# Kernel optimization log

Measured on AMD Instinct MI355X. Metric: run time of the kernel, lower is better.

Reference implementation:

```python
import jax, jax.numpy as jnp
import numpy as np

B, N, HID = 1, 2048, 1024
H, WK, WV = 16, 64, 64
DH = HID // H  # 64


def setup_inputs() -> dict:
    key = jax.random.key(0)
    ks = jax.random.split(key, 10)
    s = 0.02
    return {
        "hidden_states": jax.random.normal(ks[0], (B, N, HID), jnp.float32),
        "attention_mask": jnp.ones((B, N), jnp.float32),
        "Wq": jax.random.normal(ks[1], (HID, HID), jnp.float32) * s,
        "bq": jnp.zeros((HID,), jnp.float32),
        "Wk": jax.random.normal(ks[2], (HID, HID), jnp.float32) * s,
        "bk": jnp.zeros((HID,), jnp.float32),
        "Wv": jax.random.normal(ks[3], (HID, HID), jnp.float32) * s,
        "bv": jnp.zeros((HID,), jnp.float32),
        # Conv1D(2*WK+1, DH, bias=False): weight [nx=DH, nf=2*WK+1]
        "W_rel_k": jax.random.normal(ks[4], (DH, 2 * WK + 1), jnp.float32) * s,
        # relative_pos_val: [2*WV+1, DH]
        "W_rel_v": jax.random.normal(ks[5], (2 * WV + 1, DH), jnp.float32) * s,
    }


def _attention(hidden_states, attention_mask, Wq, bq, Wk, bk, Wv, bv, W_rel_k, W_rel_v):
    b, n, _ = hidden_states.shape

    def heads(x):  # [B,N,HID] -> [B,H,N,DH]
        return x.reshape(b, n, H, DH).transpose(0, 2, 1, 3)

    q = heads(hidden_states @ Wq + bq)
    k = heads(hidden_states @ Wk + bk)
    v = heads(hidden_states @ Wv + bv)

    scores = jnp.einsum("bhid,bhjd->bhij", q, k)  # [B,H,N,N]

    # --- relative-position key bias: bias[i, j] = q_i . w_{j-i+WK} for |j-i|<=WK ---
    a_k = jnp.einsum("bhid,dw->bhiw", q, W_rel_k)  # [B,H,N,2*WK+1]
    rows = jnp.arange(n)
    slot = rows[None, :] - rows[:, None] + WK       # [N,N] relative slot j-i+WK
    valid_k = (slot >= 0) & (slot <= 2 * WK)
    bias = a_k[:, :, rows[:, None], jnp.clip(slot, 0, 2 * WK)]  # [B,H,N,N]
    scores = scores + jnp.where(valid_k, bias, 0.0)

    scores = scores / np.float32(np.sqrt(DH))  # temperature == 1.0

    # extended attention mask: (1 - mask) * dtype_min added to scores
    ext = (1.0 - attention_mask)[:, None, None, :] * jnp.finfo(scores.dtype).min
    scores = scores + ext

    probs = jax.nn.softmax(scores, axis=-1)  # [B,H,N,N]

    ctx = jnp.einsum("bhij,bhjd->bhid", probs, v)  # [B,H,N,DH]

    # --- relative-position value: band[i, r] = probs[i, i-WV+r]; ctx += band @ W_rel_v ---
    offs = jnp.arange(2 * WV + 1)
    kpos = rows[:, None] - WV + offs[None, :]       # [N, 2*WV+1] absolute key position
    valid_v = (kpos >= 0) & (kpos < n)
    band = probs[:, :, rows[:, None], jnp.clip(kpos, 0, n - 1)]  # [B,H,N,2*WV+1]
    band = jnp.where(valid_v, band, 0.0)
    ctx = ctx + jnp.einsum("bhiw,wd->bhid", band, W_rel_v)

    # merge heads -> [B,N,HID]
    return ctx.transpose(0, 2, 1, 3).reshape(b, n, HID)


def reference(hidden_states, attention_mask, Wq, bq, Wk, bk, Wv, bv, W_rel_k, W_rel_v):
    return _attention(hidden_states, attention_mask, Wq, bq, Wk, bk, Wv, bv, W_rel_k, W_rel_v)
```

## Files before the change

### kernel.cpp

```cpp
#include <hip/hip_runtime.h>
#include <hip/hip_bf16.h>

#define NSEQ 2048
#define HIDDIM 1024
#define NH 16
#define DHEAD 64
#define NW 129
#define AKS 132

typedef float          f32x4 __attribute__((ext_vector_type(4)));
typedef _Float16       f16x4 __attribute__((ext_vector_type(4)));
typedef _Float16       f16x8 __attribute__((ext_vector_type(8)));
typedef unsigned short u16x8 __attribute__((ext_vector_type(8)));
typedef unsigned short u16;

__device__ __forceinline__ float b2f(u16 u){ return __uint_as_float(((unsigned)u) << 16); }
__device__ __forceinline__ float ld_any(const void* p, long idx, int flag){
  return flag ? b2f(((const u16*)p)[idx]) : ((const float*)p)[idx];
}

static const size_t OFF_Q    = 0;
static const size_t OFF_K    = (size_t)4  << 20;
static const size_t OFF_VT   = (size_t)8  << 20;
static const size_t OFF_WT   = (size_t)12 << 20;
static const size_t OFF_AK   = (size_t)18 << 20;
static const size_t OFF_M    = OFF_AK + (size_t)NH * NSEQ * AKS * 4;
static const size_t OFF_L    = OFF_M + (size_t)2 * NH * NSEQ * 4;
static const size_t OFF_CTXP = OFF_L + (size_t)2 * NH * NSEQ * 4;
static const size_t OFF_HSF  = OFF_CTXP + (size_t)2 * NSEQ * HIDDIM * 4;
static const size_t OFF_BIAS = OFF_HSF + (size_t)NSEQ * HIDDIM * 2;
static const size_t OFF_WRK  = OFF_BIAS + 3 * 1024 * 4;
static const size_t OFF_WRV  = OFF_WRK + (size_t)DHEAD * NW * 4;
static const size_t OFF_EXT  = OFF_WRV + (size_t)NW * DHEAD * 4;
static const size_t OFF_FLAG = OFF_EXT + (size_t)NSEQ * 4;

__global__ void detect_kernel(const unsigned* __restrict__ mask_raw, int* __restrict__ flagp){
  *flagp = (mask_raw[0] == 0x3F800000u) ? 0 : 1;
}

__global__ void cvt_hs_kernel(const void* __restrict__ hs, const int* __restrict__ flagp,
                              _Float16* __restrict__ hsf){
  const int flag = *flagp;
  const long base = (long)(blockIdx.x * 256 + threadIdx.x) * 8;
  f16x8 o;
  if (flag){
    const u16* b = (const u16*)hs;
#pragma unroll
    for (int e = 0; e < 8; e++) o[e] = (_Float16)b2f(b[base + e]);
  } else {
    const float* f = (const float*)hs;
#pragma unroll
    for (int e = 0; e < 8; e++) o[e] = (_Float16)f[base + e];
  }
  *(f16x8*)(hsf + base) = o;
}

__global__ void cvt_small_kernel(const void* __restrict__ bq, const void* __restrict__ bk,
                                 const void* __restrict__ bv, const void* __restrict__ wrk,
                                 const void* __restrict__ wrv, const void* __restrict__ mask,
                                 const int* __restrict__ flagp,
                                 float* __restrict__ biasf, float* __restrict__ wrkf,
                                 float* __restrict__ wrvf, float* __restrict__ extf){
  const int flag = *flagp;
  const int idx = blockIdx.x * 256 + threadIdx.x;
  if (idx < 1024)            biasf[idx] = ld_any(bq, idx, flag);
  else if (idx < 2048)       biasf[idx] = ld_any(bk, idx - 1024, flag);
  else if (idx < 3072)       biasf[idx] = ld_any(bv, idx - 2048, flag);
  else if (idx < 3072 + 8256)  wrkf[idx - 3072]  = ld_any(wrk, idx - 3072, flag);
  else if (idx < 3072 + 16512) wrvf[idx - 11328] = ld_any(wrv, idx - 11328, flag);
  else if (idx < 3072 + 16512 + 2048)
    extf[idx - 19584] = (1.f - ld_any(mask, idx - 19584, flag)) * -1.0e30f;
}

__global__ void wtrans_kernel(const void* __restrict__ Wq, const void* __restrict__ Wk,
                              const void* __restrict__ Wv, const int* __restrict__ flagp,
                              _Float16* __restrict__ Wt){
  __shared__ __attribute__((aligned(16))) _Float16 tile[64][65];
  const int flag = *flagp;
  const int z = blockIdx.z;
  const void* src = (z == 0) ? Wq : ((z == 1) ? Wk : Wv);
  _Float16* dst = Wt + (size_t)z * 1024 * 1024;
  const int o0 = blockIdx.x * 64, k0 = blockIdx.y * 64;
  const int t = threadIdx.x;
#pragma unroll
  for (int c = 0; c < 2; c++){
    int idx = t + 256 * c;
    int r = idx >> 3, c8 = (idx & 7) * 8;
    long off = (long)(k0 + r) * 1024 + o0 + c8;
#pragma unroll
    for (int e = 0; e < 8; e++) tile[r][c8 + e] = (_Float16)ld_any(src, off + e, flag);
  }
  __syncthreads();
#pragma unroll
  for (int c = 0; c < 2; c++){
    int idx = t + 256 * c;
    int orow = idx >> 3, k8 = (idx & 7) * 8;
    f16x8 v;
#pragma unroll
    for (int e = 0; e < 8; e++) v[e] = tile[k8 + e][orow];
    *(f16x8*)(dst + (size_t)(o0 + orow) * 1024 + k0 + k8) = v;
  }
}

__launch_bounds__(256, 2)
__global__ void qkv_kernel(const _Float16* __restrict__ hsf, const _Float16* __restrict__ Wt,
                           const float* __restrict__ biasf,
                           _Float16* __restrict__ Qf, _Float16* __restrict__ Kf,
                           _Float16* __restrict__ Vtf){
  __shared__ __attribute__((aligned(16))) _Float16 As[128 * 40];
  __shared__ __attribute__((aligned(16))) _Float16 Bs[128 * 40];
  const int z = blockIdx.z;
  const _Float16* Wz = Wt + (size_t)z * 1024 * 1024;
  const int o0 = blockIdx.x * 128, m0 = blockIdx.y * 128;
  const int t = threadIdx.x, lane = t & 63, wave = t >> 6;
  const int wm = wave >> 1, wn = wave & 1;
  const int q = lane >> 4, ln = lane & 15;
  f32x4 acc[4][4];
#pragma unroll
  for (int a = 0; a < 4; a++)
#pragma unroll
    for (int b = 0; b < 4; b++) acc[a][b] = (f32x4){0.f, 0.f, 0.f, 0.f};

  for (int k0 = 0; k0 < 1024; k0 += 32){
#pragma unroll
    for (int c = 0; c < 2; c++){
      int idx = t + 256 * c;
      int r = idx >> 2, col = (idx & 3) * 8;
      *(f16x8*)&As[r * 40 + col] = *(const f16x8*)(hsf + (size_t)(m0 + r) * 1024 + k0 + col);
      *(f16x8*)&Bs[r * 40 + col] = *(const f16x8*)(Wz + (size_t)(o0 + r) * 1024 + k0 + col);
    }
    __syncthreads();
    f16x8 af[4], bf[4];
#pragma unroll
    for (int mt = 0; mt < 4; mt++) af[mt] = *(const f16x8*)&As[(wm * 64 + mt * 16 + ln) * 40 + q * 8];
#pragma unroll
    for (int nt = 0; nt < 4; nt++) bf[nt] = *(const f16x8*)&Bs[(wn * 64 + nt * 16 + ln) * 40 + q * 8];
#pragma unroll
    for (int mt = 0; mt < 4; mt++)
#pragma unroll
      for (int nt = 0; nt < 4; nt++)
        acc[mt][nt] = __builtin_amdgcn_mfma_f32_16x16x32_f16(af[mt], bf[nt], acc[mt][nt], 0, 0, 0);
    __syncthreads();
  }
#pragma unroll
  for (int nt = 0; nt < 4; nt++){
    int o = o0 + wn * 64 + nt * 16 + ln;
    float bval = biasf[z * 1024 + o];
    int hh = o >> 6, dd = o & 63;
#pragma unroll
    for (int mt = 0; mt < 4; mt++){
      int nb = m0 + wm * 64 + mt * 16 + q * 4;
      if (z == 2){
        f16x4 pk;
#pragma unroll
        for (int r = 0; r < 4; r++) pk[r] = (_Float16)(acc[mt][nt][r] + bval);
        *(f16x4*)(Vtf + (size_t)(hh * 64 + dd) * 2048 + nb) = pk;
      } else {
        _Float16* dstp = (z == 0) ? Qf : Kf;
#pragma unroll
        for (int r = 0; r < 4; r++)
          dstp[(size_t)(hh * 2048 + nb + r) * 64 + dd] = (_Float16)(acc[mt][nt][r] + bval);
      }
    }
  }
}

__launch_bounds__(256, 2)
__global__ void ak_kernel(const _Float16* __restrict__ Qf, const float* __restrict__ wrkf,
                          float* __restrict__ ak){
  __shared__ __attribute__((aligned(16))) _Float16 WrkT[144 * 72];
  const int h = blockIdx.y;
  const int i0 = blockIdx.x * 128;
  const int t = threadIdx.x, lane = t & 63, wave = t >> 6;
  const int q = lane >> 4, ln = lane & 15;
  for (int c = 0; c < 36; c++){
    int idx = t + 256 * c;
    int w = idx >> 6, d = idx & 63;
    float v = (w < NW) ? wrkf[d * NW + w] : 0.f;
    WrkT[w * 72 + d] = (_Float16)v;
  }
  __syncthreads();
  f16x8 afr[2][2];
#pragma unroll
  for (int mt = 0; mt < 2; mt++){
    int row = i0 + wave * 32 + mt * 16 + ln;
#pragma unroll
    for (int ks = 0; ks < 2; ks++)
      afr[mt][ks] = *(const f16x8*)(Qf + (size_t)(h * 2048 + row) * 64 + ks * 32 + q * 8);
  }
  f32x4 acc[2][9];
#pragma unroll
  for (int a = 0; a < 2; a++)
#pragma unroll
    for (int b = 0; b < 9; b++) acc[a][b] = (f32x4){0.f, 0.f, 0.f, 0.f};
#pragma unroll
  for (int nt = 0; nt < 9; nt++){
    f16x8 bfr0 = *(const f16x8*)&WrkT[(nt * 16 + ln) * 72 + q * 8];
    f16x8 bfr1 = *(const f16x8*)&WrkT[(nt * 16 + ln) * 72 + 32 + q * 8];
#pragma unroll
    for (int mt = 0; mt < 2; mt++){
      acc[mt][nt] = __builtin_amdgcn_mfma_f32_16x16x32_f16(afr[mt][0], bfr0, acc[mt][nt], 0, 0, 0);
      acc[mt][nt] = __builtin_amdgcn_mfma_f32_16x16x32_f16(afr[mt][1], bfr1, acc[mt][nt], 0, 0, 0);
    }
  }
#pragma unroll
  for (int nt = 0; nt < 9; nt++){
    int w = nt * 16 + ln;
    if (w > 128) continue;
#pragma unroll
    for (int mt = 0; mt < 2; mt++){
      int ib = i0 + wave * 32 + mt * 16 + q * 4;
#pragma unroll
      for (int r = 0; r < 4; r++)
        ak[(size_t)(h * 2048 + ib + r) * AKS + w] = acc[mt][nt][r];
    }
  }
}

__launch_bounds__(256, 4)
__global__ void flash_kernel(const float* __restrict__ extf,
                             const _Float16* __restrict__ Qf, const _Float16* __restrict__ Kf,
                             const _Float16* __restrict__ Vtf, float* akm,
                             float* __restrict__ ctxpart, float* __restrict__ mws,
                             float* __restrict__ lws){
  __shared__ __attribute__((aligned(16))) _Float16 Ks[128 * 72];
  __shared__ __attribute__((aligned(16))) _Float16 Vts[64 * 136];
  __shared__ __attribute__((aligned(16))) float exts[128];
  const int h = blockIdx.x, qt = blockIdx.y, jh = blockIdx.z;
  const int t = threadIdx.x, lane = t & 63, wave = t >> 6;
  const int q = lane >> 4, ln = lane & 15;
  const int ibase = qt * 64 + wave * 16;
  const int i = ibase + ln;
  f16x8 qfrag[2];
  {
    const _Float16* qrow = Qf + (size_t)(h * 2048 + i) * 64;
    qfrag[0] = *(const f16x8*)(qrow + q * 8);
    qfrag[1] = *(const f16x8*)(qrow + 32 + q * 8);
  }
  f32x4 accc[4];
#pragma unroll
  for (int dt = 0; dt < 4; dt++) accc[dt] = (f32x4){0.f, 0.f, 0.f, 0.f};
  float m_i = -1.0e30f, l_i = 0.f;
  float* akrow = akm + (size_t)(h * 2048 + i) * AKS;

  for (int jt = 0; jt < 8; jt++){
    const int j0 = jh * 1024 + jt * 128;
#pragma unroll
    for (int c = 0; c < 4; c++){
      int idx = t + 256 * c;
      {
        int row = idx >> 3, col = idx & 7;
        *(f16x8*)&Ks[row * 72 + col * 8] =
            *(const f16x8*)(Kf + (size_t)(h * 2048 + j0 + row) * 64 + col * 8);
      }
      {
        int row = idx >> 4, col = idx & 15;
        *(f16x8*)&Vts[row * 136 + col * 8] =
            *(const f16x8*)(Vtf + (size_t)(h * 64 + row) * 2048 + j0 + col * 8);
      }
    }
    if (t < 128) exts[t] = extf[j0 + t];
    __syncthreads();
    f32x4 s[8];
#pragma unroll
    for (int mt = 0; mt < 8; mt++){
      f16x8 kf0 = *(const f16x8*)&Ks[(mt * 16 + ln) * 72 + q * 8];
      f16x8 kf1 = *(const f16x8*)&Ks[(mt * 16 + ln) * 72 + 32 + q * 8];
      f32x4 zz = (f32x4){0.f, 0.f, 0.f, 0.f};
      zz = __builtin_amdgcn_mfma_f32_16x16x32_f16(kf0, qfrag[0], zz, 0, 0, 0);
      zz = __builtin_amdgcn_mfma_f32_16x16x32_f16(kf1, qfrag[1], zz, 0, 0, 0);
      s[mt] = zz;
    }
    const bool band = (j0 <= ibase + 79) && (j0 + 127 >= ibase - 64);
#pragma unroll
    for (int mt = 0; mt < 8; mt++){
      f32x4 ev = *(const f32x4*)&exts[mt * 16 + q * 4];
#pragma unroll
      for (int r = 0; r < 4; r++){
        float x = s[mt][r];
        int w = j0 + mt * 16 + q * 4 + r - i + 64;
        if (band && (unsigned)w <= 128u){
          x = (x + akrow[w]) * 0.125f + ev[r];
          akrow[w] = x;
        } else {
          x = x * 0.125f + ev[r];
        }
        s[mt][r] = x;
      }
    }
    float tmax = -1.0e30f;
#pragma unroll
    for (int mt = 0; mt < 8; mt++)
#pragma unroll
      for (int r = 0; r < 4; r++) tmax = fmaxf(tmax, s[mt][r]);
    tmax = fmaxf(tmax, __shfl_xor(tmax, 16, 64));
    tmax = fmaxf(tmax, __shfl_xor(tmax, 32, 64));
    float mnew = fmaxf(m_i, tmax);
    float alpha = __expf(m_i - mnew);
    m_i = mnew;
    l_i *= alpha;
#pragma unroll
    for (int dt = 0; dt < 4; dt++)
#pragma unroll
      for (int r = 0; r < 4; r++) accc[dt][r] *= alpha;
    float tsum = 0.f;
    f16x4 pf[8];
#pragma unroll
    for (int mt = 0; mt < 8; mt++)
#pragma unroll
      for (int r = 0; r < 4; r++){
        float p = __expf(s[mt][r] - mnew);
        tsum += p;
        pf[mt][r] = (_Float16)p;
      }
    tsum += __shfl_xor(tsum, 16, 64);
    tsum += __shfl_xor(tsum, 32, 64);
    l_i += tsum;
#pragma unroll
    for (int dt = 0; dt < 4; dt++){
#pragma unroll
      for (int ks = 0; ks < 8; ks++){
        f16x4 vf = *(const f16x4*)&Vts[(dt * 16 + ln) * 136 + ks * 16 + q * 4];
        accc[dt] = __builtin_amdgcn_mfma_f32_16x16x16f16(vf, pf[ks], accc[dt], 0, 0, 0);
      }
    }
    __syncthreads();
  }
  float* cdst = ctxpart + (size_t)jh * NSEQ * HIDDIM;
#pragma unroll
  for (int dt = 0; dt < 4; dt++)
    *(f32x4*)(cdst + (size_t)i * 1024 + h * 64 + dt * 16 + q * 4) = accc[dt];
  if (q == 0){
    mws[jh * NH * NSEQ + h * 2048 + i] = m_i;
    lws[jh * NH * NSEQ + h * 2048 + i] = l_i;
  }
}

__launch_bounds__(256, 2)
__global__ void finish_kernel(const float* __restrict__ sband, const float* __restrict__ mws,
                              const float* __restrict__ lws, const float* __restrict__ wrvf,
                              const float* __restrict__ ctxpart, float* __restrict__ out){
  __shared__ __attribute__((aligned(16))) _Float16 WrvT[64 * 144];
  __shared__ __attribute__((aligned(16))) _Float16 pT[144 * 72];
  __shared__ __attribute__((aligned(16))) float sM[64], sIL[64], sC0[64], sC1[64];
  const int qt = blockIdx.x, h = blockIdx.y;
  const int i0 = qt * 64;
  const int t = threadIdx.x, lane = t & 63, wave = t >> 6;
  const int q = lane >> 4, ln = lane & 15;
  for (int c = 0; c < 36; c++){
    int idx = c * 256 + t;
    int w = idx >> 6, d = idx & 63;
    WrvT[d * 144 + w] = (w < NW) ? (_Float16)wrvf[w * 64 + d] : (_Float16)0.f;
  }
  if (t < 64){
    int i = i0 + t;
    float m0 = mws[h * 2048 + i],            m1 = mws[NH * NSEQ + h * 2048 + i];
    float l0 = lws[h * 2048 + i],            l1 = lws[NH * NSEQ + h * 2048 + i];
    float M = fmaxf(m0, m1);
    float a0 = __expf(m0 - M), a1 = __expf(m1 - M);
    float L = a0 * l0 + a1 * l1;
    float iL = 1.f / L;
    sM[t] = M; sIL[t] = iL; sC0[t] = a0 * iL; sC1[t] = a1 * iL;
  }
  __syncthreads();
  for (int ii = 0; ii < 16; ii++){
    int il = wave * 16 + ii;
    float Mv = sM[il], ILv = sIL[il];
    const float* srow = sband + (size_t)(h * 2048 + i0 + il) * AKS;
#pragma unroll
    for (int c = 0; c < 3; c++){
      int w = lane + 64 * c;
      if (w < 144){
        float p = (w < NW) ? __expf(srow[w] - Mv) * ILv : 0.f;
        pT[w * 72 + il] = (_Float16)p;
      }
    }
  }
  __syncthreads();
  f32x4 acc[4];
#pragma unroll
  for (int mt = 0; mt < 4; mt++) acc[mt] = (f32x4){0.f, 0.f, 0.f, 0.f};
#pragma unroll
  for (int ks = 0; ks < 9; ks++){
    f16x4 bfr;
#pragma unroll
    for (int j = 0; j < 4; j++) bfr[j] = pT[(ks * 16 + q * 4 + j) * 72 + wave * 16 + ln];
#pragma unroll
    for (int mt = 0; mt < 4; mt++){
      f16x4 afr = *(const f16x4*)&WrvT[(mt * 16 + ln) * 144 + ks * 16 + q * 4];
      acc[mt] = __builtin_amdgcn_mfma_f32_16x16x16f16(afr, bfr, acc[mt], 0, 0, 0);
    }
  }
  const int i = i0 + wave * 16 + ln;
  const float c0 = sC0[wave * 16 + ln], c1 = sC1[wave * 16 + ln];
  const float* p0 = ctxpart;
  const float* p1 = ctxpart + (size_t)NSEQ * HIDDIM;
#pragma unroll
  for (int mt = 0; mt < 4; mt++){
    size_t off = (size_t)i * 1024 + h * 64 + mt * 16 + q * 4;
    f32x4 A0 = *(const f32x4*)(p0 + off);
    f32x4 A1 = *(const f32x4*)(p1 + off);
    f32x4 o4;
#pragma unroll
    for (int r = 0; r < 4; r++) o4[r] = c0 * A0[r] + c1 * A1[r] + acc[mt][r];
    *(f32x4*)(out + off) = o4;
  }
}

extern "C" void kernel_launch(void* const* d_in, const int* in_sizes, int n_in,
                              void* d_out, int out_size, void* d_ws, size_t ws_size,
                              hipStream_t stream){
  const void* hs   = d_in[0];
  const void* mask = d_in[1];
  const void* Wq   = d_in[2];
  const void* bq   = d_in[3];
  const void* Wk   = d_in[4];
  const void* bk   = d_in[5];
  const void* Wv   = d_in[6];
  const void* bv   = d_in[7];
  const void* Wrk  = d_in[8];
  const void* Wrv  = d_in[9];
  float* out = (float*)d_out;

  char* ws = (char*)d_ws;
  _Float16* Qf    = (_Float16*)(ws + OFF_Q);
  _Float16* Kf    = (_Float16*)(ws + OFF_K);
  _Float16* Vtf   = (_Float16*)(ws + OFF_VT);
  _Float16* Wt    = (_Float16*)(ws + OFF_WT);
  float*    akp   = (float*)   (ws + OFF_AK);
  float*    mp    = (float*)   (ws + OFF_M);
  float*    lp    = (float*)   (ws + OFF_L);
  float*    ctxp  = (float*)   (ws + OFF_CTXP);
  _Float16* hsf   = (_Float16*)(ws + OFF_HSF);
  float*    biasf = (float*)   (ws + OFF_BIAS);
  float*    wrkf  = (float*)   (ws + OFF_WRK);
  float*    wrvf  = (float*)   (ws + OFF_WRV);
  float*    extf  = (float*)   (ws + OFF_EXT);
  int*      flagp = (int*)     (ws + OFF_FLAG);

  detect_kernel   <<<dim3(1),          1,   0, stream>>>((const unsigned*)mask, flagp);
  cvt_hs_kernel   <<<dim3(1024),       256, 0, stream>>>(hs, flagp, hsf);
  cvt_small_kernel<<<dim3(85),         256, 0, stream>>>(bq, bk, bv, Wrk, Wrv, mask, flagp,
                                                         biasf, wrkf, wrvf, extf);
  wtrans_kernel   <<<dim3(16, 16, 3),  256, 0, stream>>>(Wq, Wk, Wv, flagp, Wt);
  qkv_kernel      <<<dim3(8, 16, 3),   256, 0, stream>>>(hsf, Wt, biasf, Qf, Kf, Vtf);
  ak_kernel       <<<dim3(16, 16),     256, 0, stream>>>(Qf, wrkf, akp);
  flash_kernel    <<<dim3(16, 32, 2),  256, 0, stream>>>(extf, Qf, Kf, Vtf, akp, ctxp, mp, lp);
  finish_kernel   <<<dim3(32, 16),     256, 0, stream>>>(akp, mp, lp, wrvf, ctxp, out);
}
```

Baseline: 207.3 us.

## Double-buffer flash K/V tiles with direct global-to-LDS loads and XOR swizzle

Restructures the flash attention key loop to 64-key tiles, double-buffered in LDS and loaded with global_load_lds so the next tile's fetch overlaps the current tile's compute. It uses an XOR-swizzled LDS layout instead of padded rows and preloads the mask slice for the whole key half once. It also skips the accumulator rescale when no row max changed and raises wave priority around the MFMA sections. The cost is twice as many loop iterations with smaller tiles, and the code relies on the async LDS loads finishing before the barrier.

```diff
diff --git a/kernel.cpp b/kernel.cpp
--- a/kernel.cpp
+++ b/kernel.cpp
@@ -18,6 +18,10 @@
 __device__ __forceinline__ float ld_any(const void* p, long idx, int flag){
   return flag ? b2f(((const u16*)p)[idx]) : ((const float*)p)[idx];
 }
+
+#define GLOAD_LDS16(gp, lp) \
+  __builtin_amdgcn_global_load_lds((const __attribute__((address_space(1))) unsigned int*)(gp), \
+                                   (__attribute__((address_space(3))) unsigned int*)(lp), 16, 0, 0)
 
 static const size_t OFF_Q    = 0;
 static const size_t OFF_K    = (size_t)4  << 20;
@@ -223,14 +227,30 @@
                              const _Float16* __restrict__ Vtf, float* akm,
                              float* __restrict__ ctxpart, float* __restrict__ mws,
                              float* __restrict__ lws){
-  __shared__ __attribute__((aligned(16))) _Float16 Ks[128 * 72];
-  __shared__ __attribute__((aligned(16))) _Float16 Vts[64 * 136];
-  __shared__ __attribute__((aligned(16))) float exts[128];
+  __shared__ __attribute__((aligned(16))) _Float16 Ks[2 * 64 * 64];
+  __shared__ __attribute__((aligned(16))) _Float16 Vts[2 * 64 * 64];
+  __shared__ __attribute__((aligned(16))) float Exts[1024];
   const int h = blockIdx.x, qt = blockIdx.y, jh = blockIdx.z;
   const int t = threadIdx.x, lane = t & 63, wave = t >> 6;
   const int q = lane >> 4, ln = lane & 15;
   const int ibase = qt * 64 + wave * 16;
   const int i = ibase + ln;
+
+  auto stage = [&](int nb, int jn){
+#pragma unroll
+    for (int s2 = 0; s2 < 2; s2++){
+      const int g = s2 * 256 + t;
+      const int row = g >> 3, slot = g & 7;
+      const int col8 = slot ^ (row & 7);
+      const _Float16* gK = Kf + (((size_t)(h * 2048 + jn + row)) << 6) + (col8 << 3);
+      const _Float16* gV = Vtf + (((size_t)(h * 64 + row)) << 11) + jn + (col8 << 3);
+      _Float16* lK = (_Float16*)Ks + nb * 4096 + ((s2 * 4 + wave) << 9);
+      _Float16* lV = (_Float16*)Vts + nb * 4096 + ((s2 * 4 + wave) << 9);
+      GLOAD_LDS16(gK, lK);
+      GLOAD_LDS16(gV, lV);
+    }
+  };
+
   f16x8 qfrag[2];
   {
     const _Float16* qrow = Qf + (size_t)(h * 2048 + i) * 64;
@@ -243,42 +263,41 @@
   float m_i = -1.0e30f, l_i = 0.f;
   float* akrow = akm + (size_t)(h * 2048 + i) * AKS;
 
-  for (int jt = 0; jt < 8; jt++){
-    const int j0 = jh * 1024 + jt * 128;
-#pragma unroll
-    for (int c = 0; c < 4; c++){
-      int idx = t + 256 * c;
-      {
-        int row = idx >> 3, col = idx & 7;
-        *(f16x8*)&Ks[row * 72 + col * 8] =
-            *(const f16x8*)(Kf + (size_t)(h * 2048 + j0 + row) * 64 + col * 8);
-      }
-      {
-        int row = idx >> 4, col = idx & 15;
-        *(f16x8*)&Vts[row * 136 + col * 8] =
-            *(const f16x8*)(Vtf + (size_t)(h * 64 + row) * 2048 + j0 + col * 8);
-      }
-    }
-    if (t < 128) exts[t] = extf[j0 + t];
-    __syncthreads();
-    f32x4 s[8];
-#pragma unroll
-    for (int mt = 0; mt < 8; mt++){
-      f16x8 kf0 = *(const f16x8*)&Ks[(mt * 16 + ln) * 72 + q * 8];
-      f16x8 kf1 = *(const f16x8*)&Ks[(mt * 16 + ln) * 72 + 32 + q * 8];
+#pragma unroll
+  for (int c2 = 0; c2 < 4; c2++) Exts[t + 256 * c2] = extf[jh * 1024 + t + 256 * c2];
+  stage(0, jh * 1024);
+  __syncthreads();
+
+  int cur = 0;
+  for (int jt = 0; jt < 16; ++jt){
+    const int j0 = jh * 1024 + jt * 64;
+    if (jt < 15) stage(cur ^ 1, j0 + 64);
+
+    const _Float16* KsC = (const _Float16*)Ks + cur * 4096;
+    const _Float16* VsC = (const _Float16*)Vts + cur * 4096;
+
+    f32x4 s[4];
+    __builtin_amdgcn_s_setprio(1);
+#pragma unroll
+    for (int mt = 0; mt < 4; mt++){
+      const int row = mt * 16 + ln, rs = row & 7;
+      f16x8 kf0 = *(const f16x8*)&KsC[(row << 6) + ((q ^ rs) << 3)];
+      f16x8 kf1 = *(const f16x8*)&KsC[(row << 6) + (((q + 4) ^ rs) << 3)];
       f32x4 zz = (f32x4){0.f, 0.f, 0.f, 0.f};
       zz = __builtin_amdgcn_mfma_f32_16x16x32_f16(kf0, qfrag[0], zz, 0, 0, 0);
       zz = __builtin_amdgcn_mfma_f32_16x16x32_f16(kf1, qfrag[1], zz, 0, 0, 0);
       s[mt] = zz;
     }
-    const bool band = (j0 <= ibase + 79) && (j0 + 127 >= ibase - 64);
-#pragma unroll
-    for (int mt = 0; mt < 8; mt++){
-      f32x4 ev = *(const f32x4*)&exts[mt * 16 + q * 4];
+    __builtin_amdgcn_s_setprio(0);
+
+    const bool band = (j0 <= ibase + 79) && (j0 + 63 >= ibase - 64);
+#pragma unroll
+    for (int mt = 0; mt < 4; mt++){
+      f32x4 ev = *(const f32x4*)&Exts[jt * 64 + mt * 16 + (q << 2)];
 #pragma unroll
       for (int r = 0; r < 4; r++){
         float x = s[mt][r];
-        int w = j0 + mt * 16 + q * 4 + r - i + 64;
+        int w = j0 + mt * 16 + (q << 2) + r - i + 64;
         if (band && (unsigned)w <= 128u){
           x = (x + akrow[w]) * 0.125f + ev[r];
           akrow[w] = x;
@@ -288,25 +307,28 @@
         s[mt][r] = x;
       }
     }
+
     float tmax = -1.0e30f;
 #pragma unroll
-    for (int mt = 0; mt < 8; mt++)
+    for (int mt = 0; mt < 4; mt++)
 #pragma unroll
       for (int r = 0; r < 4; r++) tmax = fmaxf(tmax, s[mt][r]);
     tmax = fmaxf(tmax, __shfl_xor(tmax, 16, 64));
     tmax = fmaxf(tmax, __shfl_xor(tmax, 32, 64));
     float mnew = fmaxf(m_i, tmax);
-    float alpha = __expf(m_i - mnew);
+    if (!__all(tmax <= m_i)){
+      float alpha = __expf(m_i - mnew);
+      l_i *= alpha;
+#pragma unroll
+      for (int dt = 0; dt < 4; dt++)
+#pragma unroll
+        for (int r = 0; r < 4; r++) accc[dt][r] *= alpha;
+    }
     m_i = mnew;
-    l_i *= alpha;
-#pragma unroll
-    for (int dt = 0; dt < 4; dt++)
-#pragma unroll
-      for (int r = 0; r < 4; r++) accc[dt][r] *= alpha;
     float tsum = 0.f;
-    f16x4 pf[8];
-#pragma unroll
-    for (int mt = 0; mt < 8; mt++)
+    f16x4 pf[4];
+#pragma unroll
+    for (int mt = 0; mt < 4; mt++)
 #pragma unroll
       for (int r = 0; r < 4; r++){
         float p = __expf(s[mt][r] - mnew);
@@ -316,16 +338,24 @@
     tsum += __shfl_xor(tsum, 16, 64);
     tsum += __shfl_xor(tsum, 32, 64);
     l_i += tsum;
+
+    __builtin_amdgcn_s_setprio(1);
 #pragma unroll
     for (int dt = 0; dt < 4; dt++){
-#pragma unroll
-      for (int ks = 0; ks < 8; ks++){
-        f16x4 vf = *(const f16x4*)&Vts[(dt * 16 + ln) * 136 + ks * 16 + q * 4];
+      const int d = dt * 16 + ln, ds7 = d & 7;
+#pragma unroll
+      for (int ks = 0; ks < 4; ks++){
+        const int c8 = ((ks << 1) | (q >> 1)) ^ ds7;
+        f16x4 vf = *(const f16x4*)&VsC[(d << 6) + (c8 << 3) + ((q & 1) << 2)];
         accc[dt] = __builtin_amdgcn_mfma_f32_16x16x16f16(vf, pf[ks], accc[dt], 0, 0, 0);
       }
     }
+    __builtin_amdgcn_s_setprio(0);
+
     __syncthreads();
-  }
+    cur ^= 1;
+  }
+
   float* cdst = ctxpart + (size_t)jh * NSEQ * HIDDIM;
 #pragma unroll
   for (int dt = 0; dt < 4; dt++)
```

New measurement: 208.0 us. Within noise of the previous version (+0.4%).
